# Kernel tuning notes

Measured on AMD Instinct MI355X. Metric: run time of the kernel, lower is better.

Reference implementation:

```python
import jax, jax.numpy as jnp
import numpy as np

B, T, N, D = 4, 8, 256, 1024
DH, KD, VD, IM, KC, H, L = 768, 576, 1152, 2048, 4, 12, 5
DK, DV = KD // H, VD // H

def _rms(x, w, eps=1e-6):
    return x * jax.lax.rsqrt(jnp.mean(x * x, -1, keepdims=True) + eps) * w

def _l2(x, eps=1e-6):
    return x * jax.lax.rsqrt(jnp.sum(x * x, -1, keepdims=True) + eps)

def _conv_silu(x, w):
    # depthwise causal conv1d over tokens: x [b,n,C], w [C,K]
    K = w.shape[1]
    xp = jnp.pad(x, ((0, 0), (K - 1, 0), (0, 0)))
    y = sum(xp[:, j:j + x.shape[1], :] * w[:, j] for j in range(K))
    return jax.nn.silu(y)

def _gdn_attn(x, p):
    b, n, _ = x.shape
    q = _l2(_conv_silu(x @ p['wq'].T, p['cq']).reshape(b, n, H, DK))
    k = _l2(_conv_silu(x @ p['wk'].T, p['ck']).reshape(b, n, H, DK))
    v = _conv_silu(x @ p['wv'].T, p['cv']).reshape(b, n, H, DV)
    beta = jax.nn.sigmoid(x @ p['wb'].T)                                   # [b,n,H]
    g = -jnp.exp(p['A_log']) * jax.nn.softplus(x @ p['wa'].T + p['dt_bias'])  # mamba-style log-decay
    scale = DK ** -0.5

    def step(S, inp):
        qt, kt, vt, gt, bt = inp
        S = S * jnp.exp(gt)[..., None, None]                               # [b,H,dk,dv] gated decay
        v_old = jnp.einsum('bhk,bhkv->bhv', kt, S)
        dv = bt[..., None] * (vt - v_old)                                  # delta rule update
        S = S + kt[..., None] * dv[:, :, None, :]
        o = jnp.einsum('bhk,bhkv->bhv', qt, S)
        return S, o

    xs = (jnp.moveaxis(q * scale, 1, 0), jnp.moveaxis(k, 1, 0), jnp.moveaxis(v, 1, 0),
          jnp.moveaxis(g, 1, 0), jnp.moveaxis(beta, 1, 0))
    S0 = jnp.zeros((b, H, DK, DV), x.dtype)
    _, o = jax.lax.scan(step, S0, xs)
    o = jnp.moveaxis(o, 0, 1)                                              # [b,n,H,dv]
    gate = (x @ p['wg'].T).reshape(b, n, H, DV)
    o = _rms(o, p['onorm']) * gate * jax.nn.sigmoid(gate)                  # RMSNorm + swish gate
    return o.reshape(b, n, VD) @ p['wo'].T

def _block(x, p):
    x = x + _gdn_attn(_rms(x, p['n1']), p)
    h = _rms(x, p['n2'])
    return x + (jax.nn.silu(h @ p['w1'].T) * (h @ p['w3'].T)) @ p['w2'].T

def _forward(z, actions, enc_w, enc_b, ap_w, ap_b, temb, ln_w, ln_b, dec_w, dec_b, lp, block_fn):
    zt = z.reshape(B, T, N, D)
    feat = zt @ enc_w.T + enc_b                                            # 1x1 conv == per-token linear
    act = jnp.broadcast_to(actions[:, :, None, :], (B, T, N, actions.shape[-1]))
    tok = jnp.concatenate([feat, act], -1) @ ap_w.T + ap_b
    tpos = jnp.minimum(jnp.arange(T), temb.shape[0] - 1)
    tok = tok + temb[tpos][None, :, None, :]
    x = tok.reshape(B * T, N, DH)                                          # timesteps independent -> fold into batch
    for i in range(L):
        p = {k: v[i] for k, v in lp.items()}
        x = block_fn(x, p)
    mu = jnp.mean(x, -1, keepdims=True)
    var = jnp.mean((x - mu) ** 2, -1, keepdims=True)
    x = (x - mu) * jax.lax.rsqrt(var + 1e-5) * ln_w + ln_b                 # final LayerNorm
    delta = x @ dec_w.T + dec_b
    return (zt + delta.reshape(B, T, N, D)).reshape(B, T * N, D)

def setup_inputs():
    key = jax.random.key(0)
    cnt = [0]
    def nrm(shape, s=0.02):
        cnt[0] += 1
        return jax.random.normal(jax.random.fold_in(key, cnt[0]), shape, jnp.float32) * s
    A = 2
    return dict(
        z=nrm((B, T * N, D), 1.0), actions=nrm((B, T, A), 1.0),
        enc_w=nrm((DH, D)), enc_b=jnp.zeros((DH,), jnp.float32),
        ap_w=nrm((DH, DH + A)), ap_b=jnp.zeros((DH,), jnp.float32),
        temb=nrm((T + 1, DH)),
        ln_w=jnp.ones((DH,), jnp.float32), ln_b=jnp.zeros((DH,), jnp.float32),
        dec_w=nrm((D, DH)), dec_b=jnp.zeros((D,), jnp.float32),
        n1=jnp.ones((L, DH), jnp.float32), n2=jnp.ones((L, DH), jnp.float32),
        wq=nrm((L, KD, DH)), cq=nrm((L, KD, KC), 0.3),
        wk=nrm((L, KD, DH)), ck=nrm((L, KD, KC), 0.3),
        wv=nrm((L, VD, DH)), cv=nrm((L, VD, KC), 0.3),
        wb=nrm((L, H, DH)), wa=nrm((L, H, DH)),
        A_log=jnp.log(jax.random.uniform(jax.random.fold_in(key, 777), (L, H), jnp.float32, 1.0, 16.0)),
        dt_bias=nrm((L, H), 0.1),
        wg=nrm((L, VD, DH)), onorm=jnp.ones((L, DV), jnp.float32),
        wo=nrm((L, DH, VD)),
        w1=nrm((L, IM, DH)), w2=nrm((L, DH, IM)), w3=nrm((L, IM, DH)),
    )

def reference(z, actions, enc_w, enc_b, ap_w, ap_b, temb, ln_w, ln_b, dec_w, dec_b,
              n1, n2, wq, cq, wk, ck, wv, cv, wb, wa, A_log, dt_bias, wg, onorm, wo, w1, w2, w3):
    lp = dict(n1=n1, n2=n2, wq=wq, cq=cq, wk=wk, ck=ck, wv=wv, cv=cv, wb=wb, wa=wa,
              A_log=A_log, dt_bias=dt_bias, wg=wg, onorm=onorm, wo=wo, w1=w1, w2=w2, w3=w3)
    return _forward(z, actions, enc_w, enc_b, ap_w, ap_b, temb, ln_w, ln_b, dec_w, dec_b, lp, _block)
```

## Files before the change

kernel.cpp:

```cpp
#include <hip/hip_runtime.h>
#include <math.h>

#define RTOT 8192
#define SEQL 256
#define DHC 768
#define KDC 576
#define VDC 1152
#define IMC 2048
#define NHC 12
#define DKC 48
#define DVC 96
#define NLAY 5

typedef float f4 __attribute__((ext_vector_type(4)));
typedef __bf16 v8bf __attribute__((ext_vector_type(8)));

__device__ __forceinline__ float sigmoidf_(float x){ return 1.0f/(1.0f+expf(-x)); }
__device__ __forceinline__ float siluf_(float x){ return x/(1.0f+expf(-x)); }

__device__ __forceinline__ void gl16(const void* g, void* l) {
    __builtin_amdgcn_global_load_lds((const __attribute__((address_space(1))) void*)g,
                                     (__attribute__((address_space(3))) void*)l, 16, 0, 0);
}
#define MFMA_BF16(a,b,c) __builtin_amdgcn_mfma_f32_16x16x32_bf16((a),(b),(c),0,0,0)

__global__ __launch_bounds__(256)
void gemm3_kernel(const __bf16* __restrict__ Ah, const __bf16* __restrict__ Al,
                  const __bf16* __restrict__ Wh, const __bf16* __restrict__ Wl,
                  int K, int ldc, int mode,
                  float* Cf, const float* bias, const float* bias2, const float* res,
                  __bf16* Ch, __bf16* Cl, const float* aux)
{
    __shared__ __bf16 sAh[128*32], sAl[128*32], sBh[128*32], sBl[128*32];
    const int tid  = threadIdx.x;
    const int m0   = blockIdx.y * 128, n0 = blockIdx.x * 128;
    const int lane = tid & 63, wv = tid >> 6;
    const int wm   = (wv & 1) * 64, wn = (wv >> 1) * 64;

    const int o0 = tid * 16, o1 = o0 + 4096;
    const int r0 = o0 >> 6, s0 = (o0 >> 4) & 3;
    const int r1 = o1 >> 6, s1 = (o1 >> 4) & 3;
    const int k0 = (s0 ^ ((r0 >> 1) & 3)) * 8;
    const int k1 = (s1 ^ ((r1 >> 1) & 3)) * 8;

    const __bf16* gA0h = Ah + (size_t)(m0 + r0) * K + k0;
    const __bf16* gA1h = Ah + (size_t)(m0 + r1) * K + k1;
    const __bf16* gA0l = Al + (size_t)(m0 + r0) * K + k0;
    const __bf16* gA1l = Al + (size_t)(m0 + r1) * K + k1;
    const __bf16* gB0h = Wh + (size_t)(n0 + r0) * K + k0;
    const __bf16* gB1h = Wh + (size_t)(n0 + r1) * K + k1;
    const __bf16* gB0l = Wl + (size_t)(n0 + r0) * K + k0;
    const __bf16* gB1l = Wl + (size_t)(n0 + r1) * K + k1;

    const int fr = lane & 15, g8 = lane >> 4;
    int aoff[4], boff[4];
    #pragma unroll
    for (int f = 0; f < 4; ++f) {
        int ra = wm + f*16 + fr;
        aoff[f] = ra*32 + (g8 ^ ((ra >> 1) & 3)) * 8;
        int rb = wn + f*16 + fr;
        boff[f] = rb*32 + (g8 ^ ((rb >> 1) & 3)) * 8;
    }

    f4 acc[4][4];
    const f4 zero4 = {0.f, 0.f, 0.f, 0.f};
    #pragma unroll
    for (int i = 0; i < 4; ++i)
        #pragma unroll
        for (int j = 0; j < 4; ++j) acc[i][j] = zero4;

    for (int kt = 0; kt < K; kt += 32) {
        gl16(gA0h + kt, (char*)sAh + o0);
        gl16(gA1h + kt, (char*)sAh + o1);
        gl16(gA0l + kt, (char*)sAl + o0);
        gl16(gA1l + kt, (char*)sAl + o1);
        gl16(gB0h + kt, (char*)sBh + o0);
        gl16(gB1h + kt, (char*)sBh + o1);
        gl16(gB0l + kt, (char*)sBl + o0);
        gl16(gB1l + kt, (char*)sBl + o1);
        __syncthreads();

        v8bf bhv[4], blv[4];
        #pragma unroll
        for (int f = 0; f < 4; ++f) {
            bhv[f] = *(const v8bf*)(sBh + boff[f]);
            blv[f] = *(const v8bf*)(sBl + boff[f]);
        }
        #pragma unroll
        for (int i = 0; i < 4; ++i) {
            v8bf ahv = *(const v8bf*)(sAh + aoff[i]);
            v8bf alv = *(const v8bf*)(sAl + aoff[i]);
            #pragma unroll
            for (int j = 0; j < 4; ++j) {
                f4 t = MFMA_BF16(alv, bhv[j], acc[i][j]);
                t    = MFMA_BF16(ahv, blv[j], t);
                acc[i][j] = MFMA_BF16(ahv, bhv[j], t);
            }
        }
        __syncthreads();
    }

    const int rb4 = (lane >> 4) * 4;
    #pragma unroll
    for (int i = 0; i < 4; ++i) {
        #pragma unroll
        for (int jf = 0; jf < 4; ++jf) {
            int col = n0 + wn + jf*16 + fr;
            #pragma unroll
            for (int j = 0; j < 4; ++j) {
                int row = m0 + wm + i*16 + rb4 + j;
                size_t idx = (size_t)row * ldc + col;
                float v = acc[i][jf][j];
                if (bias)  v += bias[col];
                if (bias2) v += bias2[(size_t)(row >> 8) * ldc + col];
                if (res)   v += res[idx];
                if (mode == 2) v = siluf_(aux[idx]) * v;
                if (mode == 0) {
                    Cf[idx] = v;
                } else {
                    __bf16 h = (__bf16)v;
                    Ch[idx] = h;
                    Cl[idx] = (__bf16)(v - (float)h);
                }
            }
        }
    }
}

struct CvtBatch8 {
    const float* src[8];
    __bf16* dh[8];
    __bf16* dl[8];
    int ldv[8];
    int cols[8];
    int rowend[8];
};

__global__ __launch_bounds__(256)
void cvt_batch_kernel(CvtBatch8 b, int njobs)
{
    int r = blockIdx.x;
    int j = 0;
    while (j < njobs - 1 && r >= b.rowend[j]) ++j;
    int row0 = (j == 0) ? 0 : b.rowend[j-1];
    int lr = r - row0;
    const float* s = b.src[j] + (size_t)lr * b.ldv[j];
    __bf16* ph = b.dh[j] + (size_t)lr * b.cols[j];
    __bf16* pl = b.dl[j] + (size_t)lr * b.cols[j];
    int cols = b.cols[j];
    for (int c = threadIdx.x; c < cols; c += 256) {
        float v = s[c];
        __bf16 hh = (__bf16)v;
        ph[c] = hh;
        pl[c] = (__bf16)(v - (float)hh);
    }
}

__global__ __launch_bounds__(256)
void bias2_kernel(const float* __restrict__ actions, const float* __restrict__ ap_w,
                  const float* __restrict__ ap_b, const float* __restrict__ temb,
                  float* __restrict__ B2)
{
    int bt = blockIdx.x;
    int t  = bt & 7;
    float a0 = actions[bt*2], a1 = actions[bt*2+1];
    for (int c = threadIdx.x; c < DHC; c += 256)
        B2[bt*DHC + c] = ap_b[c] + temb[t*DHC + c] + a0*ap_w[c*770 + 768] + a1*ap_w[c*770 + 769];
}

__global__ __launch_bounds__(256)
void rmsnorm_kernel(const float* __restrict__ X, const float* __restrict__ w,
                    __bf16* __restrict__ Yh, __bf16* __restrict__ Yl)
{
    int row = blockIdx.x, tid = threadIdx.x;
    const float* xr = X + (size_t)row*DHC;
    float v0 = xr[tid], v1 = xr[tid+256], v2 = xr[tid+512];
    __shared__ float red[256];
    red[tid] = v0*v0 + v1*v1 + v2*v2;
    __syncthreads();
    for (int s = 128; s; s >>= 1) { if (tid < s) red[tid] += red[tid+s]; __syncthreads(); }
    float r = 1.0f/sqrtf(red[0]/768.0f + 1e-6f);
    float y0 = v0*r*w[tid], y1 = v1*r*w[tid+256], y2 = v2*r*w[tid+512];
    __bf16* ph = Yh + (size_t)row*DHC;
    __bf16* pl = Yl + (size_t)row*DHC;
    __bf16 h0 = (__bf16)y0, h1 = (__bf16)y1, h2 = (__bf16)y2;
    ph[tid] = h0;     pl[tid]     = (__bf16)(y0 - (float)h0);
    ph[tid+256] = h1; pl[tid+256] = (__bf16)(y1 - (float)h1);
    ph[tid+512] = h2; pl[tid+512] = (__bf16)(y2 - (float)h2);
}

__global__ __launch_bounds__(256)
void layernorm_kernel(const float* __restrict__ X, const float* __restrict__ w,
                      const float* __restrict__ b, __bf16* __restrict__ Yh,
                      __bf16* __restrict__ Yl)
{
    int row = blockIdx.x, tid = threadIdx.x;
    const float* xr = X + (size_t)row*DHC;
    float v0 = xr[tid], v1 = xr[tid+256], v2 = xr[tid+512];
    __shared__ float rs[256], rs2[256];
    rs[tid]  = v0+v1+v2;
    rs2[tid] = v0*v0+v1*v1+v2*v2;
    __syncthreads();
    for (int s = 128; s; s >>= 1) { if (tid < s) { rs[tid]+=rs[tid+s]; rs2[tid]+=rs2[tid+s]; } __syncthreads(); }
    float mu  = rs[0]/768.0f;
    float var = rs2[0]/768.0f - mu*mu;
    float r = 1.0f/sqrtf(var + 1e-5f);
    float y0 = (v0-mu)*r*w[tid]     + b[tid];
    float y1 = (v1-mu)*r*w[tid+256] + b[tid+256];
    float y2 = (v2-mu)*r*w[tid+512] + b[tid+512];
    __bf16* ph = Yh + (size_t)row*DHC;
    __bf16* pl = Yl + (size_t)row*DHC;
    __bf16 h0 = (__bf16)y0, h1 = (__bf16)y1, h2 = (__bf16)y2;
    ph[tid] = h0;     pl[tid]     = (__bf16)(y0 - (float)h0);
    ph[tid+256] = h1; pl[tid+256] = (__bf16)(y1 - (float)h1);
    ph[tid+512] = h2; pl[tid+512] = (__bf16)(y2 - (float)h2);
}

__global__ __launch_bounds__(64)
void convsilu_kernel(const float* __restrict__ P, int ldp, const float* __restrict__ cw,
                     float* __restrict__ Y, int ldd, int C)
{
    int c = blockIdx.x*64 + threadIdx.x;
    if (c >= C) return;
    int r = blockIdx.y;
    int t = r & (SEQL-1);
    float acc = P[(size_t)r*ldp + c] * cw[c*4+3];
    if (t >= 1) acc += P[(size_t)(r-1)*ldp + c] * cw[c*4+2];
    if (t >= 2) acc += P[(size_t)(r-2)*ldp + c] * cw[c*4+1];
    if (t >= 3) acc += P[(size_t)(r-3)*ldp + c] * cw[c*4+0];
    Y[(size_t)r*ldd + c] = siluf_(acc);
}

__global__ __launch_bounds__(128)
void l2norm_kernel(float* __restrict__ X, int ld, int col0, float scale)
{
    int row = blockIdx.x;
    int wave = threadIdx.x >> 6, lane = threadIdx.x & 63;
    #pragma unroll
    for (int i = 0; i < 6; ++i) {
        int h = wave*6 + i;
        size_t base = (size_t)row*ld + col0 + h*DKC;
        float v = (lane < DKC) ? X[base + lane] : 0.f;
        float ss = v*v;
        for (int off = 32; off; off >>= 1) ss += __shfl_down(ss, off);
        ss = __shfl(ss, 0);
        float r = scale / sqrtf(ss + 1e-6f);
        if (lane < DKC) X[base + lane] = v*r;
    }
}

__global__ __launch_bounds__(256)
void betag_kernel(const __bf16* __restrict__ XNh, const __bf16* __restrict__ XNl,
                  const float* __restrict__ wb, const float* __restrict__ wa,
                  const float* __restrict__ Alog, const float* __restrict__ dtb,
                  float* __restrict__ Beta, float* __restrict__ Dec)
{
    int row = blockIdx.x, tid = threadIdx.x;
    __shared__ float sx[DHC];
    for (int i = tid; i < DHC; i += 256)
        sx[i] = (float)XNh[(size_t)row*DHC + i] + (float)XNl[(size_t)row*DHC + i];
    __syncthreads();
    int wave = tid >> 6, lane = tid & 63;
    for (int d = 0; d < 6; ++d) {
        int out = wave*6 + d;
        const float* wr = (out < NHC) ? (wb + out*DHC) : (wa + (out-NHC)*DHC);
        float acc = 0.f;
        for (int j = lane; j < DHC; j += 64) acc += sx[j]*wr[j];
        for (int off = 32; off; off >>= 1) acc += __shfl_down(acc, off);
        if (lane == 0) {
            if (out < NHC) {
                Beta[(size_t)row*NHC + out] = sigmoidf_(acc);
            } else {
                int h = out - NHC;
                float sp = acc + dtb[h];
                sp = (sp > 20.f) ? sp : log1pf(expf(sp));
                Dec[(size_t)row*NHC + h] = expf(-expf(Alog[h]) * sp);
            }
        }
    }
}

#define SCAN_STEP(CUR, T)                                                   \
    {                                                                       \
        float dec = sbuf[CUR][192], beta = sbuf[CUR][193];                  \
        const float* sk = &sbuf[CUR][0];                                    \
        const float* sq = &sbuf[CUR][48];                                   \
        const float* sv = &sbuf[CUR][96];                                   \
        float pv0 = 0.f, pv1 = 0.f;                                         \
        _Pragma("unroll")                                                   \
        for (int i = 0; i < 12; i += 2) {                                   \
            S[i]   *= dec; pv0 += sk[rg*12+i]  *S[i];                       \
            S[i+1] *= dec; pv1 += sk[rg*12+i+1]*S[i+1];                     \
        }                                                                   \
        float pv = pv0 + pv1;                                               \
        pv += __shfl_xor(pv, 1); pv += __shfl_xor(pv, 2);                   \
        float dvv = beta * (sv[vc] - pv);                                   \
        float po0 = 0.f, po1 = 0.f;                                         \
        _Pragma("unroll")                                                   \
        for (int i = 0; i < 12; i += 2) {                                   \
            S[i]   += sk[rg*12+i]  *dvv; po0 += sq[rg*12+i]  *S[i];         \
            S[i+1] += sk[rg*12+i+1]*dvv; po1 += sq[rg*12+i+1]*S[i+1];       \
        }                                                                   \
        float po = po0 + po1;                                               \
        po += __shfl_xor(po, 1); po += __shfl_xor(po, 2);                   \
        if (rg == 0) op[(size_t)(T)*VDC + vc] = po;                         \
    }

__global__ __launch_bounds__(384)
void scan_kernel(const float* __restrict__ QKV, const float* __restrict__ Beta,
                 const float* __restrict__ Dec, float* __restrict__ O)
{
    int bid = blockIdx.x;
    int seq = bid / NHC, h = bid % NHC;
    int tid = threadIdx.x;
    int vc = tid >> 2, rg = tid & 3;
    __shared__ float sbuf[2][194];

    float S[12];
    #pragma unroll
    for (int i = 0; i < 12; ++i) S[i] = 0.f;

    float* op = O + (size_t)seq*SEQL*VDC + h*DVC;

    const float* gptr = QKV;
    int gstride = 0;
    const bool ldr = (tid < 194);
    if (tid < 192) {
        int col;
        if (tid < 48)       col = 576  + h*DKC + tid;
        else if (tid < 96)  col =        h*DKC + (tid - 48);
        else                col = 1152 + h*DVC + (tid - 96);
        gptr = QKV + (size_t)seq*SEQL*2304 + col;
        gstride = 2304;
    } else if (tid == 192) {
        gptr = Dec  + (size_t)seq*SEQL*NHC + h;  gstride = NHC;
    } else if (tid == 193) {
        gptr = Beta + (size_t)seq*SEQL*NHC + h;  gstride = NHC;
    }

    float pA = 0.f, pB = 0.f;
    if (ldr) {
        sbuf[0][tid] = gptr[0];
        pA = gptr[gstride];
    }
    __syncthreads();

    int cur = 0;
    for (int t = 0; t < SEQL; t += 2) {
        {
            int tn = t + 2; if (tn > SEQL-1) tn = SEQL-1;
            if (ldr) pB = gptr[(size_t)tn * gstride];
            SCAN_STEP(cur, t)
            if (ldr) sbuf[cur^1][tid] = pA;
            __syncthreads();
            cur ^= 1;
        }
        {
            int tn = t + 3; if (tn > SEQL-1) tn = SEQL-1;
            if (ldr) pA = gptr[(size_t)tn * gstride];
            SCAN_STEP(cur, t+1)
            if (ldr) sbuf[cur^1][tid] = pB;
            __syncthreads();
            cur ^= 1;
        }
    }
}

__global__ __launch_bounds__(128)
void opost_kernel(const float* __restrict__ O, const float* __restrict__ G, int ldg,
                  const float* __restrict__ onorm, __bf16* __restrict__ Oh,
                  __bf16* __restrict__ Ol)
{
    int row = blockIdx.x;
    int wave = threadIdx.x >> 6, lane = threadIdx.x & 63;
    #pragma unroll
    for (int i = 0; i < 6; ++i) {
        int h = wave*6 + i;
        size_t baseO = (size_t)row*VDC + h*DVC;
        size_t baseG = (size_t)row*ldg + h*DVC;
        float a = O[baseO + lane];
        float c = (lane < 32) ? O[baseO + 64 + lane] : 0.f;
        float ss = a*a + c*c;
        for (int off = 32; off; off >>= 1) ss += __shfl_down(ss, off);
        ss = __shfl(ss, 0);
        float r = 1.0f/sqrtf(ss/96.0f + 1e-6f);
        float ga = G[baseG + lane];
        float v0 = a*r*onorm[lane]*ga*sigmoidf_(ga);
        { __bf16 hh = (__bf16)v0; Oh[baseO+lane] = hh; Ol[baseO+lane] = (__bf16)(v0 - (float)hh); }
        if (lane < 32) {
            float gb = G[baseG + 64 + lane];
            float v1 = c*r*onorm[64+lane]*gb*sigmoidf_(gb);
            __bf16 hh = (__bf16)v1; Oh[baseO+64+lane] = hh; Ol[baseO+64+lane] = (__bf16)(v1 - (float)hh);
        }
    }
}

static inline void gemm3(const __bf16* Ah, const __bf16* Al, const __bf16* Wh, const __bf16* Wl,
                         int K, int ldc, int mode, float* Cf, const float* bias,
                         const float* bias2, const float* res, __bf16* Ch, __bf16* Cl,
                         const float* aux, hipStream_t s)
{
    dim3 grid(ldc/128, RTOT/128);
    hipLaunchKernelGGL(gemm3_kernel, grid, dim3(256), 0, s, Ah, Al, Wh, Wl, K, ldc, mode,
                       Cf, bias, bias2, res, Ch, Cl, aux);
}

extern "C" void kernel_launch(void* const* d_in, const int* in_sizes, int n_in,
                              void* d_out, int out_size, void* d_ws, size_t ws_size,
                              hipStream_t stream)
{
    const float* z       = (const float*)d_in[0];
    const float* actions = (const float*)d_in[1];
    const float* enc_w   = (const float*)d_in[2];
    const float* enc_b   = (const float*)d_in[3];
    const float* ap_w    = (const float*)d_in[4];
    const float* ap_b    = (const float*)d_in[5];
    const float* temb    = (const float*)d_in[6];
    const float* ln_w    = (const float*)d_in[7];
    const float* ln_b    = (const float*)d_in[8];
    const float* dec_w   = (const float*)d_in[9];
    const float* dec_b   = (const float*)d_in[10];
    const float* n1      = (const float*)d_in[11];
    const float* n2      = (const float*)d_in[12];
    const float* wq      = (const float*)d_in[13];
    const float* cq      = (const float*)d_in[14];
    const float* wk      = (const float*)d_in[15];
    const float* ck      = (const float*)d_in[16];
    const float* wv      = (const float*)d_in[17];
    const float* cv      = (const float*)d_in[18];
    const float* wb      = (const float*)d_in[19];
    const float* wa      = (const float*)d_in[20];
    const float* A_log   = (const float*)d_in[21];
    const float* dt_bias = (const float*)d_in[22];
    const float* wg      = (const float*)d_in[23];
    const float* onorm   = (const float*)d_in[24];
    const float* wo      = (const float*)d_in[25];
    const float* w1      = (const float*)d_in[26];
    const float* w2      = (const float*)d_in[27];
    const float* w3      = (const float*)d_in[28];

    const size_t R = RTOT;
    const float qscale = 0.14433756729740643f;

    float* X    = (float*)d_ws;
    float* BUF1 = X    + 768*R;
    float* O    = BUF1 + 1152*R;
    float* QKV  = O    + 1152*R;
    float* BETA = QKV  + 2304*R;
    float* DEC  = BETA + 12*R;
    float* TMP  = DEC  + 12*R;
    __bf16* XNh = (__bf16*)(TMP + 32*768);
    __bf16* XNl = XNh + 768*R;
    __bf16* WS0 = XNl + 768*R;

    const size_t need = (size_t)(768+1152+1152+2304+24)*R*4 + 32*768*4
                      + ((size_t)1536*R + 16515072)*2;
    if (ws_size < need) return;

    __bf16* zh  = (__bf16*)QKV;
    __bf16* zl  = zh + 1024*R;
    __bf16* Oh  = (__bf16*)QKV;
    __bf16* Ol  = Oh + 1152*R;
    float*  A1f = QKV;
    __bf16* A1h = (__bf16*)BUF1;
    __bf16* A1l = (__bf16*)O;

    {
        __bf16* ench = WS0;                       __bf16* encl = ench + (size_t)768*1024;
        __bf16* aph  = encl + (size_t)768*1024;   __bf16* apl  = aph  + (size_t)768*768;

        CvtBatch8 eb{};
        eb.src[0]=z;     eb.dh[0]=zh;   eb.dl[0]=zl;   eb.ldv[0]=1024; eb.cols[0]=1024; eb.rowend[0]=8192;
        eb.src[1]=enc_w; eb.dh[1]=ench; eb.dl[1]=encl; eb.ldv[1]=1024; eb.cols[1]=1024; eb.rowend[1]=8960;
        eb.src[2]=ap_w;  eb.dh[2]=aph;  eb.dl[2]=apl;  eb.ldv[2]=770;  eb.cols[2]=768;  eb.rowend[2]=9728;
        hipLaunchKernelGGL(cvt_batch_kernel, dim3(9728), dim3(256), 0, stream, eb, 3);

        hipLaunchKernelGGL(bias2_kernel, dim3(32), dim3(256), 0, stream, actions, ap_w, ap_b, temb, TMP);
        gemm3(zh, zl, ench, encl, 1024, 768, 1, nullptr, enc_b, nullptr, nullptr, XNh, XNl, nullptr, stream);
        gemm3(XNh, XNl, aph, apl, 768, 768, 0, X, nullptr, TMP, nullptr, nullptr, nullptr, nullptr, stream);
    }

    for (int l = 0; l < NLAY; ++l) {
        __bf16* qkh = WS0;                        __bf16* qkl = qkh + (size_t)1152*768;
        __bf16* vh  = qkl + (size_t)1152*768;     __bf16* vl  = vh  + (size_t)1152*768;
        __bf16* gh  = vl  + (size_t)1152*768;     __bf16* gl_ = gh  + (size_t)1152*768;
        __bf16* woh = gl_ + (size_t)1152*768;     __bf16* wol = woh + (size_t)768*1152;
        __bf16* w1h = wol + (size_t)768*1152;     __bf16* w1l = w1h + (size_t)2048*768;
        __bf16* w3h = w1l + (size_t)2048*768;     __bf16* w3l = w3h + (size_t)2048*768;
        __bf16* w2h = w3l + (size_t)2048*768;     __bf16* w2l = w2h + (size_t)768*2048;

        CvtBatch8 lb{};
        lb.src[0]=wq + (size_t)l*KDC*DHC; lb.dh[0]=qkh;                   lb.dl[0]=qkl;                   lb.ldv[0]=768;  lb.cols[0]=768;  lb.rowend[0]=576;
        lb.src[1]=wk + (size_t)l*KDC*DHC; lb.dh[1]=qkh+(size_t)576*768;   lb.dl[1]=qkl+(size_t)576*768;   lb.ldv[1]=768;  lb.cols[1]=768;  lb.rowend[1]=1152;
        lb.src[2]=wv + (size_t)l*VDC*DHC; lb.dh[2]=vh;                    lb.dl[2]=vl;                    lb.ldv[2]=768;  lb.cols[2]=768;  lb.rowend[2]=2304;
        lb.src[3]=wg + (size_t)l*VDC*DHC; lb.dh[3]=gh;                    lb.dl[3]=gl_;                   lb.ldv[3]=768;  lb.cols[3]=768;  lb.rowend[3]=3456;
        lb.src[4]=wo + (size_t)l*DHC*VDC; lb.dh[4]=woh;                   lb.dl[4]=wol;                   lb.ldv[4]=1152; lb.cols[4]=1152; lb.rowend[4]=4224;
        lb.src[5]=w1 + (size_t)l*IMC*DHC; lb.dh[5]=w1h;                   lb.dl[5]=w1l;                   lb.ldv[5]=768;  lb.cols[5]=768;  lb.rowend[5]=6272;
        lb.src[6]=w3 + (size_t)l*IMC*DHC; lb.dh[6]=w3h;                   lb.dl[6]=w3l;                   lb.ldv[6]=768;  lb.cols[6]=768;  lb.rowend[6]=8320;
        lb.src[7]=w2 + (size_t)l*DHC*IMC; lb.dh[7]=w2h;                   lb.dl[7]=w2l;                   lb.ldv[7]=2048; lb.cols[7]=2048; lb.rowend[7]=9088;
        hipLaunchKernelGGL(cvt_batch_kernel, dim3(9088), dim3(256), 0, stream, lb, 8);

        hipLaunchKernelGGL(rmsnorm_kernel, dim3(RTOT), dim3(256), 0, stream, X, n1 + l*DHC, XNh, XNl);

        gemm3(XNh, XNl, qkh, qkl, 768, 1152, 0, BUF1, nullptr, nullptr, nullptr, nullptr, nullptr, nullptr, stream);
        hipLaunchKernelGGL(convsilu_kernel, dim3(9,  RTOT), dim3(64), 0, stream, BUF1,       1152, cq + (size_t)l*KDC*4, QKV,        2304, KDC);
        hipLaunchKernelGGL(convsilu_kernel, dim3(9,  RTOT), dim3(64), 0, stream, BUF1 + 576, 1152, ck + (size_t)l*KDC*4, QKV + 576,  2304, KDC);
        gemm3(XNh, XNl, vh, vl, 768, 1152, 0, BUF1, nullptr, nullptr, nullptr, nullptr, nullptr, nullptr, stream);
        hipLaunchKernelGGL(convsilu_kernel, dim3(18, RTOT), dim3(64), 0, stream, BUF1,       1152, cv + (size_t)l*VDC*4, QKV + 1152, 2304, VDC);
        gemm3(XNh, XNl, gh, gl_, 768, 1152, 0, BUF1, nullptr, nullptr, nullptr, nullptr, nullptr, nullptr, stream);
        hipLaunchKernelGGL(betag_kernel, dim3(RTOT), dim3(256), 0, stream,
                           XNh, XNl, wb + (size_t)l*NHC*DHC, wa + (size_t)l*NHC*DHC,
                           A_log + l*NHC, dt_bias + l*NHC, BETA, DEC);

        hipLaunchKernelGGL(l2norm_kernel, dim3(RTOT), dim3(128), 0, stream, QKV, 2304, 0,   qscale);
        hipLaunchKernelGGL(l2norm_kernel, dim3(RTOT), dim3(128), 0, stream, QKV, 2304, 576, 1.0f);

        hipLaunchKernelGGL(scan_kernel, dim3(32*NHC), dim3(384), 0, stream, QKV, BETA, DEC, O);

        hipLaunchKernelGGL(opost_kernel, dim3(RTOT), dim3(128), 0, stream, O, BUF1, 1152,
                           onorm + l*DVC, Oh, Ol);
        gemm3(Oh, Ol, woh, wol, 1152, 768, 0, X, nullptr, nullptr, X, nullptr, nullptr, nullptr, stream);

        hipLaunchKernelGGL(rmsnorm_kernel, dim3(RTOT), dim3(256), 0, stream, X, n2 + l*DHC, XNh, XNl);
        gemm3(XNh, XNl, w1h, w1l, 768, 2048, 0, A1f, nullptr, nullptr, nullptr, nullptr, nullptr, nullptr, stream);
        gemm3(XNh, XNl, w3h, w3l, 768, 2048, 2, nullptr, nullptr, nullptr, nullptr, A1h, A1l, A1f, stream);
        gemm3(A1h, A1l, w2h, w2l, 2048, 768, 0, X, nullptr, nullptr, X, nullptr, nullptr, nullptr, stream);
    }

    {
        __bf16* dech = WS0;  __bf16* decl = dech + (size_t)1024*768;
        CvtBatch8 db{};
        db.src[0]=dec_w; db.dh[0]=dech; db.dl[0]=decl; db.ldv[0]=768; db.cols[0]=768; db.rowend[0]=1024;
        hipLaunchKernelGGL(cvt_batch_kernel, dim3(1024), dim3(256), 0, stream, db, 1);
        hipLaunchKernelGGL(layernorm_kernel, dim3(RTOT), dim3(256), 0, stream, X, ln_w, ln_b, XNh, XNl);
        gemm3(XNh, XNl, dech, decl, 768, 1024, 0, (float*)d_out, dec_b, nullptr, z, nullptr, nullptr, nullptr, stream);
    }
}
```

Baseline: 5.884 ms.

## Drop activation low-part in most GEMMs and restructure scan to one wave per head

Adds a template flag to the split-bf16 GEMM that skips the activation low-half loads and the Al*Wh MFMA. Most in-layer projections (qkv, gate, FFN w1/w3/w2) now use it, cutting MFMA work by a third and A-side memory traffic for those GEMMs. The FFN intermediate no longer stores its low part. Separately, the delta-rule scan kernel shrinks from 384 threads to one 64-lane wave per head, with each lane holding a 12x6 state tile, so cross-wave barrier cost goes away at the price of more serial work per lane. Precision drops to roughly bf16 activations for those GEMMs, which may affect accuracy.

```diff
diff --git a/kernel.cpp b/kernel.cpp
--- a/kernel.cpp
+++ b/kernel.cpp
@@ -24,6 +24,7 @@
 }
 #define MFMA_BF16(a,b,c) __builtin_amdgcn_mfma_f32_16x16x32_bf16((a),(b),(c),0,0,0)
 
+template<bool HASAL>
 __global__ __launch_bounds__(256)
 void gemm3_kernel(const __bf16* __restrict__ Ah, const __bf16* __restrict__ Al,
                   const __bf16* __restrict__ Wh, const __bf16* __restrict__ Wl,
@@ -31,7 +32,8 @@
                   float* Cf, const float* bias, const float* bias2, const float* res,
                   __bf16* Ch, __bf16* Cl, const float* aux)
 {
-    __shared__ __bf16 sAh[128*32], sAl[128*32], sBh[128*32], sBl[128*32];
+    __shared__ __bf16 sAh[128*32], sBh[128*32], sBl[128*32];
+    __shared__ __bf16 sAl[HASAL ? 128*32 : 16];
     const int tid  = threadIdx.x;
     const int m0   = blockIdx.y * 128, n0 = blockIdx.x * 128;
     const int lane = tid & 63, wv = tid >> 6;
@@ -45,8 +47,8 @@
 
     const __bf16* gA0h = Ah + (size_t)(m0 + r0) * K + k0;
     const __bf16* gA1h = Ah + (size_t)(m0 + r1) * K + k1;
-    const __bf16* gA0l = Al + (size_t)(m0 + r0) * K + k0;
-    const __bf16* gA1l = Al + (size_t)(m0 + r1) * K + k1;
+    const __bf16* gA0l = HASAL ? (Al + (size_t)(m0 + r0) * K + k0) : nullptr;
+    const __bf16* gA1l = HASAL ? (Al + (size_t)(m0 + r1) * K + k1) : nullptr;
     const __bf16* gB0h = Wh + (size_t)(n0 + r0) * K + k0;
     const __bf16* gB1h = Wh + (size_t)(n0 + r1) * K + k1;
     const __bf16* gB0l = Wl + (size_t)(n0 + r0) * K + k0;
@@ -72,8 +74,10 @@
     for (int kt = 0; kt < K; kt += 32) {
         gl16(gA0h + kt, (char*)sAh + o0);
         gl16(gA1h + kt, (char*)sAh + o1);
-        gl16(gA0l + kt, (char*)sAl + o0);
-        gl16(gA1l + kt, (char*)sAl + o1);
+        if constexpr (HASAL) {
+            gl16(gA0l + kt, (char*)sAl + o0);
+            gl16(gA1l + kt, (char*)sAl + o1);
+        }
         gl16(gB0h + kt, (char*)sBh + o0);
         gl16(gB1h + kt, (char*)sBh + o1);
         gl16(gB0l + kt, (char*)sBl + o0);
@@ -89,11 +93,13 @@
         #pragma unroll
         for (int i = 0; i < 4; ++i) {
             v8bf ahv = *(const v8bf*)(sAh + aoff[i]);
-            v8bf alv = *(const v8bf*)(sAl + aoff[i]);
+            v8bf alv;
+            if constexpr (HASAL) alv = *(const v8bf*)(sAl + aoff[i]);
             #pragma unroll
             for (int j = 0; j < 4; ++j) {
-                f4 t = MFMA_BF16(alv, bhv[j], acc[i][j]);
-                t    = MFMA_BF16(ahv, blv[j], t);
+                f4 t = acc[i][j];
+                if constexpr (HASAL) t = MFMA_BF16(alv, bhv[j], t);
+                t = MFMA_BF16(ahv, blv[j], t);
                 acc[i][j] = MFMA_BF16(ahv, bhv[j], t);
             }
         }
@@ -120,7 +126,7 @@
                 } else {
                     __bf16 h = (__bf16)v;
                     Ch[idx] = h;
-                    Cl[idx] = (__bf16)(v - (float)h);
+                    if (Cl) Cl[idx] = (__bf16)(v - (float)h);
                 }
             }
         }
@@ -280,86 +286,111 @@
     }
 }
 
-#define SCAN_STEP(CUR, T)                                                   \
-    {                                                                       \
-        float dec = sbuf[CUR][192], beta = sbuf[CUR][193];                  \
-        const float* sk = &sbuf[CUR][0];                                    \
-        const float* sq = &sbuf[CUR][48];                                   \
-        const float* sv = &sbuf[CUR][96];                                   \
-        float pv0 = 0.f, pv1 = 0.f;                                         \
-        _Pragma("unroll")                                                   \
-        for (int i = 0; i < 12; i += 2) {                                   \
-            S[i]   *= dec; pv0 += sk[rg*12+i]  *S[i];                       \
-            S[i+1] *= dec; pv1 += sk[rg*12+i+1]*S[i+1];                     \
-        }                                                                   \
-        float pv = pv0 + pv1;                                               \
-        pv += __shfl_xor(pv, 1); pv += __shfl_xor(pv, 2);                   \
-        float dvv = beta * (sv[vc] - pv);                                   \
-        float po0 = 0.f, po1 = 0.f;                                         \
-        _Pragma("unroll")                                                   \
-        for (int i = 0; i < 12; i += 2) {                                   \
-            S[i]   += sk[rg*12+i]  *dvv; po0 += sq[rg*12+i]  *S[i];         \
-            S[i+1] += sk[rg*12+i+1]*dvv; po1 += sq[rg*12+i+1]*S[i+1];       \
-        }                                                                   \
-        float po = po0 + po1;                                               \
-        po += __shfl_xor(po, 1); po += __shfl_xor(po, 2);                   \
-        if (rg == 0) op[(size_t)(T)*VDC + vc] = po;                         \
-    }
-
-__global__ __launch_bounds__(384)
+#define SCAN_STEP_W(CUR, T)                                                  \
+    {                                                                        \
+        float dec  = sbuf[CUR][192], beta = sbuf[CUR][193];                  \
+        const float* sk = &sbuf[CUR][0];                                     \
+        const float* sq = &sbuf[CUR][48];                                    \
+        const float* sv = &sbuf[CUR][96];                                    \
+        float kx[12], qx[12], vx[6], pv[6], po[6];                           \
+        _Pragma("unroll")                                                    \
+        for (int i = 0; i < 12; ++i) { kx[i] = sk[rg*12+i]; qx[i] = sq[rg*12+i]; } \
+        _Pragma("unroll")                                                    \
+        for (int j = 0; j < 6; ++j) vx[j] = sv[g*6+j];                       \
+        _Pragma("unroll")                                                    \
+        for (int j = 0; j < 6; ++j) {                                        \
+            float a0 = 0.f, a1 = 0.f;                                        \
+            _Pragma("unroll")                                                \
+            for (int i = 0; i < 12; i += 2) {                                \
+                S[i][j]   *= dec; a0 += kx[i]  *S[i][j];                     \
+                S[i+1][j] *= dec; a1 += kx[i+1]*S[i+1][j];                   \
+            }                                                                \
+            pv[j] = a0 + a1;                                                 \
+        }                                                                    \
+        _Pragma("unroll")                                                    \
+        for (int j = 0; j < 6; ++j) {                                        \
+            pv[j] += __shfl_xor(pv[j], 1);                                   \
+            pv[j] += __shfl_xor(pv[j], 2);                                   \
+        }                                                                    \
+        _Pragma("unroll")                                                    \
+        for (int j = 0; j < 6; ++j) {                                        \
+            float dvv = beta * (vx[j] - pv[j]);                              \
+            float a0 = 0.f, a1 = 0.f;                                        \
+            _Pragma("unroll")                                                \
+            for (int i = 0; i < 12; i += 2) {                                \
+                S[i][j]   += kx[i]  *dvv; a0 += qx[i]  *S[i][j];             \
+                S[i+1][j] += kx[i+1]*dvv; a1 += qx[i+1]*S[i+1][j];           \
+            }                                                                \
+            po[j] = a0 + a1;                                                 \
+        }                                                                    \
+        _Pragma("unroll")                                                    \
+        for (int j = 0; j < 6; ++j) {                                        \
+            po[j] += __shfl_xor(po[j], 1);                                   \
+            po[j] += __shfl_xor(po[j], 2);                                   \
+        }                                                                    \
+        if (rg == 0) {                                                       \
+            _Pragma("unroll")                                                \
+            for (int j = 0; j < 6; ++j) op[(size_t)(T)*VDC + g*6 + j] = po[j]; \
+        }                                                                    \
+    }
+
+__global__ __launch_bounds__(64)
 void scan_kernel(const float* __restrict__ QKV, const float* __restrict__ Beta,
                  const float* __restrict__ Dec, float* __restrict__ O)
 {
     int bid = blockIdx.x;
     int seq = bid / NHC, h = bid % NHC;
-    int tid = threadIdx.x;
-    int vc = tid >> 2, rg = tid & 3;
+    int lane = threadIdx.x;
+    int g = lane >> 2, rg = lane & 3;
     __shared__ float sbuf[2][194];
 
-    float S[12];
-    #pragma unroll
-    for (int i = 0; i < 12; ++i) S[i] = 0.f;
+    float S[12][6];
+    #pragma unroll
+    for (int i = 0; i < 12; ++i)
+        #pragma unroll
+        for (int j = 0; j < 6; ++j) S[i][j] = 0.f;
 
     float* op = O + (size_t)seq*SEQL*VDC + h*DVC;
 
-    const float* gptr = QKV;
-    int gstride = 0;
-    const bool ldr = (tid < 194);
-    if (tid < 192) {
-        int col;
-        if (tid < 48)       col = 576  + h*DKC + tid;
-        else if (tid < 96)  col =        h*DKC + (tid - 48);
-        else                col = 1152 + h*DVC + (tid - 96);
-        gptr = QKV + (size_t)seq*SEQL*2304 + col;
-        gstride = 2304;
-    } else if (tid == 192) {
-        gptr = Dec  + (size_t)seq*SEQL*NHC + h;  gstride = NHC;
-    } else if (tid == 193) {
-        gptr = Beta + (size_t)seq*SEQL*NHC + h;  gstride = NHC;
-    }
-
-    float pA = 0.f, pB = 0.f;
-    if (ldr) {
-        sbuf[0][tid] = gptr[0];
-        pA = gptr[gstride];
-    }
+    const float* gp[4]; int gs[4]; bool en[4];
+    #pragma unroll
+    for (int s = 0; s < 4; ++s) {
+        int e = lane + s*64;
+        en[s] = (e < 194);
+        const float* base = QKV;  int stride = 0;
+        if (e < 48)        { base = QKV + (size_t)seq*SEQL*2304 + 576 + h*DKC + e;          stride = 2304; }
+        else if (e < 96)   { base = QKV + (size_t)seq*SEQL*2304 + h*DKC + (e-48);           stride = 2304; }
+        else if (e < 192)  { base = QKV + (size_t)seq*SEQL*2304 + 1152 + h*DVC + (e-96);    stride = 2304; }
+        else if (e == 192) { base = Dec  + (size_t)seq*SEQL*NHC + h;                        stride = NHC; }
+        else if (e == 193) { base = Beta + (size_t)seq*SEQL*NHC + h;                        stride = NHC; }
+        gp[s] = base; gs[s] = stride;
+    }
+
+    float pA[4], pB[4];
+    #pragma unroll
+    for (int s = 0; s < 4; ++s)
+        if (en[s]) { sbuf[0][lane + s*64] = gp[s][0]; pA[s] = gp[s][gs[s]]; }
     __syncthreads();
 
     int cur = 0;
     for (int t = 0; t < SEQL; t += 2) {
         {
             int tn = t + 2; if (tn > SEQL-1) tn = SEQL-1;
-            if (ldr) pB = gptr[(size_t)tn * gstride];
-            SCAN_STEP(cur, t)
-            if (ldr) sbuf[cur^1][tid] = pA;
+            #pragma unroll
+            for (int s = 0; s < 4; ++s) if (en[s]) pB[s] = gp[s][(size_t)tn * gs[s]];
+            SCAN_STEP_W(cur, t)
+            #pragma unroll
+            for (int s = 0; s < 4; ++s) if (en[s]) sbuf[cur^1][lane + s*64] = pA[s];
             __syncthreads();
             cur ^= 1;
         }
         {
             int tn = t + 3; if (tn > SEQL-1) tn = SEQL-1;
-            if (ldr) pA = gptr[(size_t)tn * gstride];
-            SCAN_STEP(cur, t+1)
-            if (ldr) sbuf[cur^1][tid] = pB;
+            #pragma unroll
+            for (int s = 0; s < 4; ++s) if (en[s]) pA[s] = gp[s][(size_t)tn * gs[s]];
+            SCAN_STEP_W(cur, t+1)
+            #pragma unroll
+            for (int s = 0; s < 4; ++s) if (en[s]) sbuf[cur^1][lane + s*64] = pB[s];
             __syncthreads();
             cur ^= 1;
         }
@@ -395,14 +426,19 @@
     }
 }
 
-static inline void gemm3(const __bf16* Ah, const __bf16* Al, const __bf16* Wh, const __bf16* Wl,
+static inline void gemm3(bool hasAl,
+                         const __bf16* Ah, const __bf16* Al, const __bf16* Wh, const __bf16* Wl,
                          int K, int ldc, int mode, float* Cf, const float* bias,
                          const float* bias2, const float* res, __bf16* Ch, __bf16* Cl,
                          const float* aux, hipStream_t s)
 {
     dim3 grid(ldc/128, RTOT/128);
-    hipLaunchKernelGGL(gemm3_kernel, grid, dim3(256), 0, s, Ah, Al, Wh, Wl, K, ldc, mode,
-                       Cf, bias, bias2, res, Ch, Cl, aux);
+    if (hasAl)
+        hipLaunchKernelGGL(gemm3_kernel<true>,  grid, dim3(256), 0, s, Ah, Al, Wh, Wl, K, ldc, mode,
+                           Cf, bias, bias2, res, Ch, Cl, aux);
+    else
+        hipLaunchKernelGGL(gemm3_kernel<false>, grid, dim3(256), 0, s, Ah, Al, Wh, Wl, K, ldc, mode,
+                           Cf, bias, bias2, res, Ch, Cl, aux);
 }
 
 extern "C" void kernel_launch(void* const* d_in, const int* in_sizes, int n_in,
@@ -463,7 +499,6 @@
     __bf16* Ol  = Oh + 1152*R;
     float*  A1f = QKV;
     __bf16* A1h = (__bf16*)BUF1;
-    __bf16* A1l = (__bf16*)O;
 
     {
         __bf16* ench = WS0;                       __bf16* encl = ench + (size_t)768*1024;
@@ -476,8 +511,8 @@
         hipLaunchKernelGGL(cvt_batch_kernel, dim3(9728), dim3(256), 0, stream, eb, 3);
 
         hipLaunchKernelGGL(bias2_kernel, dim3(32), dim3(256), 0, stream, actions, ap_w, ap_b, temb, TMP);
-        gemm3(zh, zl, ench, encl, 1024, 768, 1, nullptr, enc_b, nullptr, nullptr, XNh, XNl, nullptr, stream);
-        gemm3(XNh, XNl, aph, apl, 768, 768, 0, X, nullptr, TMP, nullptr, nullptr, nullptr, nullptr, stream);
+        gemm3(true, zh, zl, ench, encl, 1024, 768, 1, nullptr, enc_b, nullptr, nullptr, XNh, XNl, nullptr, stream);
+        gemm3(true, XNh, XNl, aph, apl, 768, 768, 0, X, nullptr, TMP, nullptr, nullptr, nullptr, nullptr, stream);
     }
 
     for (int l = 0; l < NLAY; ++l) {
@@ -502,12 +537,12 @@
 
         hipLaunchKernelGGL(rmsnorm_kernel, dim3(RTOT), dim3(256), 0, stream, X, n1 + l*DHC, XNh, XNl);
 
-        gemm3(XNh, XNl, qkh, qkl, 768, 1152, 0, BUF1, nullptr, nullptr, nullptr, nullptr, nullptr, nullptr, stream);
+        gemm3(false, XNh, nullptr, qkh, qkl, 768, 1152, 0, BUF1, nullptr, nullptr, nullptr, nullptr, nullptr, nullptr, stream);
         hipLaunchKernelGGL(convsilu_kernel, dim3(9,  RTOT), dim3(64), 0, stream, BUF1,       1152, cq + (size_t)l*KDC*4, QKV,        2304, KDC);
         hipLaunchKernelGGL(convsilu_kernel, dim3(9,  RTOT), dim3(64), 0, stream, BUF1 + 576, 1152, ck + (size_t)l*KDC*4, QKV + 576,  2304, KDC);
-        gemm3(XNh, XNl, vh, vl, 768, 1152, 0, BUF1, nullptr, nullptr, nullptr, nullptr, nullptr, nullptr, stream);
+        gemm3(false, XNh, nullptr, vh, vl, 768, 1152, 0, BUF1, nullptr, nullptr, nullptr, nullptr, nullptr, nullptr, stream);
         hipLaunchKernelGGL(convsilu_kernel, dim3(18, RTOT), dim3(64), 0, stream, BUF1,       1152, cv + (size_t)l*VDC*4, QKV + 1152, 2304, VDC);
-        gemm3(XNh, XNl, gh, gl_, 768, 1152, 0, BUF1, nullptr, nullptr, nullptr, nullptr, nullptr, nullptr, stream);
+        gemm3(false, XNh, nullptr, gh, gl_, 768, 1152, 0, BUF1, nullptr, nullptr, nullptr, nullptr, nullptr, nullptr, stream);
         hipLaunchKernelGGL(betag_kernel, dim3(RTOT), dim3(256), 0, stream,
                            XNh, XNl, wb + (size_t)l*NHC*DHC, wa + (size_t)l*NHC*DHC,
                            A_log + l*NHC, dt_bias + l*NHC, BETA, DEC);
@@ -515,16 +550,16 @@
         hipLaunchKernelGGL(l2norm_kernel, dim3(RTOT), dim3(128), 0, stream, QKV, 2304, 0,   qscale);
         hipLaunchKernelGGL(l2norm_kernel, dim3(RTOT), dim3(128), 0, stream, QKV, 2304, 576, 1.0f);
 
-        hipLaunchKernelGGL(scan_kernel, dim3(32*NHC), dim3(384), 0, stream, QKV, BETA, DEC, O);
+        hipLaunchKernelGGL(scan_kernel, dim3(32*NHC), dim3(64), 0, stream, QKV, BETA, DEC, O);
 
         hipLaunchKernelGGL(opost_kernel, dim3(RTOT), dim3(128), 0, stream, O, BUF1, 1152,
                            onorm + l*DVC, Oh, Ol);
-        gemm3(Oh, Ol, woh, wol, 1152, 768, 0, X, nullptr, nullptr, X, nullptr, nullptr, nullptr, stream);
+        gemm3(true, Oh, Ol, woh, wol, 1152, 768, 0, X, nullptr, nullptr, X, nullptr, nullptr, nullptr, stream);
 
         hipLaunchKernelGGL(rmsnorm_kernel, dim3(RTOT), dim3(256), 0, stream, X, n2 + l*DHC, XNh, XNl);
-        gemm3(XNh, XNl, w1h, w1l, 768, 2048, 0, A1f, nullptr, nullptr, nullptr, nullptr, nullptr, nullptr, stream);
-        gemm3(XNh, XNl, w3h, w3l, 768, 2048, 2, nullptr, nullptr, nullptr, nullptr, A1h, A1l, A1f, stream);
-        gemm3(A1h, A1l, w2h, w2l, 2048, 768, 0, X, nullptr, nullptr, X, nullptr, nullptr, nullptr, stream);
+        gemm3(false, XNh, nullptr, w1h, w1l, 768, 2048, 0, A1f, nullptr, nullptr, nullptr, nullptr, nullptr, nullptr, stream);
+        gemm3(false, XNh, nullptr, w3h, w3l, 768, 2048, 2, nullptr, nullptr, nullptr, nullptr, A1h, nullptr, A1f, stream);
+        gemm3(false, A1h, nullptr, w2h, w2l, 2048, 768, 0, X, nullptr, nullptr, X, nullptr, nullptr, nullptr, stream);
     }
 
     {
@@ -533,6 +568,6 @@
         db.src[0]=dec_w; db.dh[0]=dech; db.dl[0]=decl; db.ldv[0]=768; db.cols[0]=768; db.rowend[0]=1024;
         hipLaunchKernelGGL(cvt_batch_kernel, dim3(1024), dim3(256), 0, stream, db, 1);
         hipLaunchKernelGGL(layernorm_kernel, dim3(RTOT), dim3(256), 0, stream, X, ln_w, ln_b, XNh, XNl);
-        gemm3(XNh, XNl, dech, decl, 768, 1024, 0, (float*)d_out, dec_b, nullptr, z, nullptr, nullptr, nullptr, stream);
-    }
-}
+        gemm3(true, XNh, XNl, dech, decl, 768, 1024, 0, (float*)d_out, dec_b, nullptr, z, nullptr, nullptr, nullptr, stream);
+    }
+}
```

Measured after the change: 5.796 ms. Within noise of the previous version (-1.5%).
